# Performance work log

Measured on AMD Instinct MI355X. Metric: run time of the kernel, lower is better.

## Reference

```python
import jax, jax.numpy as jnp
import numpy as np

R = 3.0            # search_range
EPS = 0.01         # forward_backward_error
UPD_MULT = 1.0     # UPDATE_MULTIPLIER_THRESHOLD


def _clamp(coords, H, W):
    # coords [..., 2] = (x, y); clamp x to [0, W-1], y to [0, H-1]
    return jnp.stack([jnp.clip(coords[..., 0], 0.0, W - 1.0),
                      jnp.clip(coords[..., 1], 0.0, H - 1.0)], axis=-1)


def _scores(coords, corr_flat):
    # coords [B,H,W,2] (x,y); corr_flat [B*H*W, Hc, Wc]; bilinear sample one scalar per pixel
    B, H, W, _ = coords.shape
    N, Hc, Wc = corr_flat.shape
    c = coords.reshape(-1, 2)
    x, y = c[:, 0], c[:, 1]
    x0 = jnp.floor(x); y0 = jnp.floor(y)
    wx = x - x0; wy = y - y0
    x0i = jnp.clip(x0.astype(jnp.int32), 0, Wc - 1)
    x1i = jnp.clip(x0i + 1, 0, Wc - 1)
    y0i = jnp.clip(y0.astype(jnp.int32), 0, Hc - 1)
    y1i = jnp.clip(y0i + 1, 0, Hc - 1)
    n = jnp.arange(N)
    v00 = corr_flat[n, y0i, x0i]; v01 = corr_flat[n, y0i, x1i]
    v10 = corr_flat[n, y1i, x0i]; v11 = corr_flat[n, y1i, x1i]
    s = (v00 * (1 - wx) * (1 - wy) + v01 * wx * (1 - wy)
         + v10 * (1 - wx) * wy + v11 * wx * wy)
    return s.reshape(B, H, W)


def _propagate(coords, corr_flat, dxy):
    # PatchMatch propagation step along direction (dx, dy): take neighbor's match
    # shifted by the same pixel offset if it scores higher.
    dx, dy = dxy
    B, H, W, _ = coords.shape
    best = coords
    best_s = _scores(best, corr_flat)
    cand_h = _clamp(jnp.roll(coords, dx, axis=2) + jnp.array([dx, 0.0], coords.dtype), H, W)
    cand_v = _clamp(jnp.roll(coords, dy, axis=1) + jnp.array([0.0, dy], coords.dtype), H, W)
    for cand in (cand_h, cand_v):
        s = _scores(cand, corr_flat)
        upd = s > best_s
        best = jnp.where(upd[..., None], cand, best)
        best_s = jnp.maximum(s, best_s)
    return best


def _random_search(coords, corr_flat, key):
    B, H, W, _ = coords.shape
    new = _clamp(coords + R * jax.random.normal(key, coords.shape, coords.dtype), H, W)
    old_s = _scores(coords, corr_flat)
    new_s = _scores(new, corr_flat)
    upd = (new_s - UPD_MULT * old_s) > 0
    return jnp.where(upd[..., None], new, coords)


def _handle(matching, corr_flat, key):
    coords = jnp.transpose(matching, (0, 2, 3, 1))  # [B,H,W,2]
    k1, k2, k3 = jax.random.split(key, 3)
    res = _propagate(coords, corr_flat, (1, 1))
    res = _random_search(res, corr_flat, k1)
    res = _propagate(res, corr_flat, (-1, -1))
    res = _random_search(res, corr_flat, k2)
    res = _propagate(res, corr_flat, (-1, 1))
    res = _random_search(res, corr_flat, k3)
    res = _propagate(res, corr_flat, (1, -1))
    return res


def _bilinear_map(img, coords):
    # img [B,H,W,C] sampled at coords [B,H,W,2] (x,y) -> [B,H,W,C]
    B, H, W, C = img.shape
    def per_b(im, co):
        x = co[..., 0].reshape(-1); y = co[..., 1].reshape(-1)
        x0 = jnp.floor(x); y0 = jnp.floor(y)
        wx = (x - x0)[:, None]; wy = (y - y0)[:, None]
        x0i = jnp.clip(x0.astype(jnp.int32), 0, W - 1)
        x1i = jnp.clip(x0i + 1, 0, W - 1)
        y0i = jnp.clip(y0.astype(jnp.int32), 0, H - 1)
        y1i = jnp.clip(y0i + 1, 0, H - 1)
        v00 = im[y0i, x0i]; v01 = im[y0i, x1i]
        v10 = im[y1i, x0i]; v11 = im[y1i, x1i]
        out = (v00 * (1 - wx) * (1 - wy) + v01 * wx * (1 - wy)
               + v10 * (1 - wx) * wy + v11 * wx * wy)
        return out.reshape(H, W, C)
    return jax.vmap(per_b)(img, coords)


def setup_inputs() -> dict:
    key = jax.random.key(0)
    k1, k2, k3 = jax.random.split(key, 3)
    B, H, W = 4, 64, 64
    # matching fields: absolute (x, y) coords in-range
    mf = jax.random.uniform(k1, (B, 2, H, W), jnp.float32)
    mb = jax.random.uniform(k2, (B, 2, H, W), jnp.float32)
    scale = jnp.array([W - 1.0, H - 1.0], jnp.float32).reshape(1, 2, 1, 1)
    matching_f = mf * scale
    matching_b = mb * scale
    corr_map = jax.random.normal(k3, (B, H, W, H, W), jnp.float32)
    return {"matching_f": matching_f, "matching_b": matching_b, "corr_map": corr_map}


def reference(matching_f, matching_b, corr_map):
    B, H, W = corr_map.shape[0], corr_map.shape[1], corr_map.shape[2]
    corr_f = corr_map.reshape(B * H * W, H, W)
    # backward direction samples the transposed correlation volume
    corr_b = jnp.transpose(corr_map, (0, 3, 4, 1, 2)).reshape(B * H * W, H, W)
    key = jax.random.key(42)
    kf, kb = jax.random.split(key)
    res_f = _handle(matching_f, corr_f, kf)   # [B,H,W,2]
    res_b = _handle(matching_b, corr_b, kb)   # [B,H,W,2]
    # forward-backward consistency: sample backward field at forward matches
    counter = _bilinear_map(res_b, res_f)
    diff = jnp.max(jnp.abs(res_f - counter), axis=-1)
    invalid = (diff > EPS)[..., None]
    res = jnp.where(invalid, jnp.transpose(matching_f, (0, 2, 3, 1)), res_f)
    return jnp.transpose(res, (0, 3, 1, 2))
```

## Files before the change

### kernel.cpp

```cpp
#include <hip/hip_runtime.h>
#include <stdint.h>

#pragma clang fp contract(off)

__host__ __device__ inline void tf2x32(uint32_t k0, uint32_t k1,
                                       uint32_t x0, uint32_t x1,
                                       uint32_t* o0, uint32_t* o1) {
  const uint32_t ks2 = k0 ^ k1 ^ 0x1BD11BDAu;
  x0 += k0; x1 += k1;
#define TF_R(r) { x0 += x1; x1 = (x1 << (r)) | (x1 >> (32 - (r))); x1 ^= x0; }
  TF_R(13) TF_R(15) TF_R(26) TF_R(6)
  x0 += k1;  x1 += ks2 + 1u;
  TF_R(17) TF_R(29) TF_R(16) TF_R(24)
  x0 += ks2; x1 += k0 + 2u;
  TF_R(13) TF_R(15) TF_R(26) TF_R(6)
  x0 += k0;  x1 += k1 + 3u;
  TF_R(17) TF_R(29) TF_R(16) TF_R(24)
  x0 += k1;  x1 += ks2 + 4u;
  TF_R(13) TF_R(15) TF_R(26) TF_R(6)
  x0 += ks2; x1 += k0 + 5u;
#undef TF_R
  *o0 = x0; *o1 = x1;
}

__device__ inline float erfinv_xla(float x) {
#pragma clang fp contract(off)
  float w = -log1pf(-(x * x));
  float p;
  if (w < 5.0f) {
    w = w - 2.5f;
    p = 2.81022636e-08f;
    p = 3.43273939e-07f  + p * w;
    p = -3.5233877e-06f  + p * w;
    p = -4.39150654e-06f + p * w;
    p = 0.00021858087f   + p * w;
    p = -0.00125372503f  + p * w;
    p = -0.00417768164f  + p * w;
    p = 0.246640727f     + p * w;
    p = 1.50140941f      + p * w;
  } else {
    w = sqrtf(w) - 3.0f;
    p = -0.000200214257f;
    p = 0.000100950558f  + p * w;
    p = 0.00134934322f   + p * w;
    p = -0.00367342844f  + p * w;
    p = 0.00573950773f   + p * w;
    p = -0.0076224613f   + p * w;
    p = 0.00943887047f   + p * w;
    p = 1.00167406f      + p * w;
    p = 2.83297682f      + p * w;
  }
  return p * x;
}

__device__ inline float jax_normal(uint32_t k0, uint32_t k1, uint32_t idx) {
#pragma clang fp contract(off)
  uint32_t o0, o1;
  tf2x32(k0, k1, 0u, idx, &o0, &o1);
  uint32_t bits = o0 ^ o1;
  float f = __uint_as_float((bits >> 9) | 0x3f800000u) - 1.0f;
  float u = f * 2.0f + (-0x1.fffffep-1f);
  u = fmaxf(-0x1.fffffep-1f, u);
  return 0x1.6a09e6p+0f * erfinv_xla(u);
}

__device__ inline float score_at(const float* __restrict__ base, int stride,
                                 float x, float y) {
#pragma clang fp contract(off)
  float x0 = floorf(x), y0 = floorf(y);
  float wx = x - x0, wy = y - y0;
  int xi = (int)x0; xi = xi < 0 ? 0 : (xi > 63 ? 63 : xi);
  int yi = (int)y0; yi = yi < 0 ? 0 : (yi > 63 ? 63 : yi);
  int x1 = xi + 1 > 63 ? 63 : xi + 1;
  int y1 = yi + 1 > 63 ? 63 : yi + 1;
  float v00 = base[(yi * 64 + xi) * stride];
  float v01 = base[(yi * 64 + x1) * stride];
  float v10 = base[(y1 * 64 + xi) * stride];
  float v11 = base[(y1 * 64 + x1) * stride];
  float omx = 1.0f - wx, omy = 1.0f - wy;
  return (((v00 * omx) * omy + (v01 * wx) * omy) + (v10 * omx) * wy) + (v11 * wx) * wy;
}

__global__ __launch_bounds__(64) void step_kernel(
    const float* __restrict__ mf, const float* __restrict__ mb,
    const float4* __restrict__ in_c, float4* __restrict__ out_c,
    const float* __restrict__ corr, int dx, int dy,
    uint32_t k0f, uint32_t k1f, uint32_t k0b, uint32_t k1b,
    int do_rs, int from_matching) {
#pragma clang fp contract(off)
  int g = (int)(blockIdx.x * 64 + threadIdx.x);
  int dir = g >> 14, b = (g >> 12) & 3, p = g & 4095;
  int i = p >> 6, j = p & 63;

  const float* base; int stride;
  if (dir == 0) { base = corr + (size_t)(b * 4096 + p) * 4096; stride = 1; }
  else          { base = corr + (size_t)b * 16777216 + p;      stride = 4096; }

  int jh = (j - dx) & 63;
  int iv = (i - dy) & 63;

  float2 bst; float bs;
  float2 ch, cv;
  if (from_matching) {
    const float* m = dir ? mb : mf;
    float2 c = make_float2(m[((b * 2 + 0) * 64 + i) * 64 + j],
                           m[((b * 2 + 1) * 64 + i) * 64 + j]);
    ch = make_float2(m[((b * 2 + 0) * 64 + i ) * 64 + jh], m[((b * 2 + 1) * 64 + i ) * 64 + jh]);
    cv = make_float2(m[((b * 2 + 0) * 64 + iv) * 64 + j ], m[((b * 2 + 1) * 64 + iv) * 64 + j ]);
    bst = c;
    bs = score_at(base, stride, c.x, c.y);
  } else {
    const float4* ic = in_c + dir * 16384 + b * 4096;
    float4 own = ic[p];
    float4 nh  = ic[(i << 6) | jh];
    float4 nv  = ic[(iv << 6) | j];
    bst = make_float2(own.x, own.y);
    bs  = own.z;
    ch = make_float2(nh.x, nh.y);
    cv = make_float2(nv.x, nv.y);
  }
  ch.x = fminf(fmaxf(ch.x + (float)dx, 0.0f), 63.0f);
  cv.y = fminf(fmaxf(cv.y + (float)dy, 0.0f), 63.0f);

  float sh = score_at(base, stride, ch.x, ch.y);
  float sv = score_at(base, stride, cv.x, cv.y);
  if (sh > bs) bst = ch;
  bs = fmaxf(sh, bs);
  if (sv > bs) bst = cv;
  bs = fmaxf(sv, bs);

  if (do_rs) {
    uint32_t kk0 = dir ? k0b : k0f, kk1 = dir ? k1b : k1f;
    uint32_t pg = (uint32_t)(b * 4096 + p);
    float n0 = jax_normal(kk0, kk1, 2u * pg);
    float n1 = jax_normal(kk0, kk1, 2u * pg + 1u);
    float nx = fminf(fmaxf(bst.x + 3.0f * n0, 0.0f), 63.0f);
    float ny = fminf(fmaxf(bst.y + 3.0f * n1, 0.0f), 63.0f);
    float sn = score_at(base, stride, nx, ny);
    if (sn - bs > 0.0f) { bst = make_float2(nx, ny); bs = sn; }
  }
  out_c[dir * 16384 + b * 4096 + p] = make_float4(bst.x, bst.y, bs, 0.0f);
}

__global__ __launch_bounds__(256) void combine_kernel(const float* __restrict__ mf,
                                                      const float4* __restrict__ res,
                                                      float* __restrict__ out) {
#pragma clang fp contract(off)
  int pg = (int)(blockIdx.x * 256 + threadIdx.x);
  int b = pg >> 12, hw = pg & 4095;
  int i = hw >> 6, j = hw & 63;
  float4 rf4 = res[pg];
  float2 rf = make_float2(rf4.x, rf4.y);
  const float4* rb = res + 16384 + b * 4096;
  float x0 = floorf(rf.x), y0 = floorf(rf.y);
  float wx = rf.x - x0, wy = rf.y - y0;
  int xi = (int)x0; xi = xi < 0 ? 0 : (xi > 63 ? 63 : xi);
  int yi = (int)y0; yi = yi < 0 ? 0 : (yi > 63 ? 63 : yi);
  int x1 = xi + 1 > 63 ? 63 : xi + 1;
  int y1 = yi + 1 > 63 ? 63 : yi + 1;
  float4 v00 = rb[yi * 64 + xi], v01 = rb[yi * 64 + x1];
  float4 v10 = rb[y1 * 64 + xi], v11 = rb[y1 * 64 + x1];
  float omx = 1.0f - wx, omy = 1.0f - wy;
  float c0 = (((v00.x * omx) * omy + (v01.x * wx) * omy) + (v10.x * omx) * wy) + (v11.x * wx) * wy;
  float c1 = (((v00.y * omx) * omy + (v01.y * wx) * omy) + (v10.y * omx) * wy) + (v11.y * wx) * wy;
  float d = fmaxf(fabsf(rf.x - c0), fabsf(rf.y - c1));
  bool invalid = d > 0.01f;
  out[((b * 2 + 0) * 64 + i) * 64 + j] = invalid ? mf[((b * 2 + 0) * 64 + i) * 64 + j] : rf.x;
  out[((b * 2 + 1) * 64 + i) * 64 + j] = invalid ? mf[((b * 2 + 1) * 64 + i) * 64 + j] : rf.y;
}

extern "C" void kernel_launch(void* const* d_in, const int* in_sizes, int n_in,
                              void* d_out, int out_size, void* d_ws, size_t ws_size,
                              hipStream_t stream) {
  const float* mf   = (const float*)d_in[0];
  const float* mb   = (const float*)d_in[1];
  const float* corr = (const float*)d_in[2];
  float* out  = (float*)d_out;
  float4* bufA = (float4*)d_ws;
  float4* bufB = bufA + 32768;

  uint32_t kf0, kf1, kb0, kb1, K[12];
  tf2x32(0u, 42u, 0u, 0u, &kf0, &kf1);
  tf2x32(0u, 42u, 0u, 1u, &kb0, &kb1);
  for (uint32_t s = 0; s < 3; ++s) {
    tf2x32(kf0, kf1, 0u, s, &K[0 + s * 2], &K[0 + s * 2 + 1]);
    tf2x32(kb0, kb1, 0u, s, &K[6 + s * 2], &K[6 + s * 2 + 1]);
  }

  dim3 grid(512), block(64);
  step_kernel<<<grid, block, 0, stream>>>(mf, mb, nullptr, bufA, corr,  1,  1,
                                          K[0], K[1], K[6], K[7], 1, 1);
  step_kernel<<<grid, block, 0, stream>>>(mf, mb, bufA, bufB, corr, -1, -1,
                                          K[2], K[3], K[8], K[9], 1, 0);
  step_kernel<<<grid, block, 0, stream>>>(mf, mb, bufB, bufA, corr, -1,  1,
                                          K[4], K[5], K[10], K[11], 1, 0);
  step_kernel<<<grid, block, 0, stream>>>(mf, mb, bufA, bufB, corr,  1, -1,
                                          0u, 0u, 0u, 0u, 0, 0);
  combine_kernel<<<dim3(64), dim3(256), 0, stream>>>(mf, bufB, out);
  (void)in_sizes; (void)n_in; (void)out_size; (void)ws_size;
}
```

Measured before the change: 333.9 us.

## Fuse four propagation steps into one tiled kernel with halo recompute

Replaces the four sequential step kernel launches with a single kernel. Each 64-thread block handles an 8x8 tile and recomputes a shrinking halo (11x11, 10x10, 9x9) in shared memory, so the propagation stages need no global round trips or extra launches. This removes three launches and the intermediate buffer traffic. In exchange it does redundant scoring and RNG work on the halo pixels (121+100+81 vs 64 per stage), all of which do random gathers from the correlation volume. The intermediate result also shrinks from float4 to float2 for the combine step.

```diff
diff --git a/kernel.cpp b/kernel.cpp
--- a/kernel.cpp
+++ b/kernel.cpp
@@ -81,85 +81,141 @@
   return (((v00 * omx) * omy + (v01 * wx) * omy) + (v10 * omx) * wy) + (v11 * wx) * wy;
 }
 
-__global__ __launch_bounds__(64) void step_kernel(
-    const float* __restrict__ mf, const float* __restrict__ mb,
-    const float4* __restrict__ in_c, float4* __restrict__ out_c,
-    const float* __restrict__ corr, int dx, int dy,
-    uint32_t k0f, uint32_t k1f, uint32_t k0b, uint32_t k1b,
-    int do_rs, int from_matching) {
-#pragma clang fp contract(off)
-  int g = (int)(blockIdx.x * 64 + threadIdx.x);
-  int dir = g >> 14, b = (g >> 12) & 3, p = g & 4095;
-  int i = p >> 6, j = p & 63;
-
-  const float* base; int stride;
-  if (dir == 0) { base = corr + (size_t)(b * 4096 + p) * 4096; stride = 1; }
-  else          { base = corr + (size_t)b * 16777216 + p;      stride = 4096; }
-
-  int jh = (j - dx) & 63;
-  int iv = (i - dy) & 63;
-
-  float2 bst; float bs;
-  float2 ch, cv;
-  if (from_matching) {
-    const float* m = dir ? mb : mf;
-    float2 c = make_float2(m[((b * 2 + 0) * 64 + i) * 64 + j],
-                           m[((b * 2 + 1) * 64 + i) * 64 + j]);
-    ch = make_float2(m[((b * 2 + 0) * 64 + i ) * 64 + jh], m[((b * 2 + 1) * 64 + i ) * 64 + jh]);
-    cv = make_float2(m[((b * 2 + 0) * 64 + iv) * 64 + j ], m[((b * 2 + 1) * 64 + iv) * 64 + j ]);
-    bst = c;
-    bs = score_at(base, stride, c.x, c.y);
-  } else {
-    const float4* ic = in_c + dir * 16384 + b * 4096;
-    float4 own = ic[p];
-    float4 nh  = ic[(i << 6) | jh];
-    float4 nv  = ic[(iv << 6) | j];
-    bst = make_float2(own.x, own.y);
-    bs  = own.z;
-    ch = make_float2(nh.x, nh.y);
-    cv = make_float2(nv.x, nv.y);
-  }
-  ch.x = fminf(fmaxf(ch.x + (float)dx, 0.0f), 63.0f);
-  cv.y = fminf(fmaxf(cv.y + (float)dy, 0.0f), 63.0f);
-
-  float sh = score_at(base, stride, ch.x, ch.y);
-  float sv = score_at(base, stride, cv.x, cv.y);
-  if (sh > bs) bst = ch;
+__device__ inline float4 prop_rs(float2 own, float own_s, float2 nh, float2 nv,
+                                 float fdx, float fdy,
+                                 const float* __restrict__ base, int stride,
+                                 bool do_rs, uint32_t k0, uint32_t k1,
+                                 uint32_t pg) {
+#pragma clang fp contract(off)
+  float chx = fminf(fmaxf(nh.x + fdx, 0.0f), 63.0f);
+  float chy = nh.y;
+  float cvx = nv.x;
+  float cvy = fminf(fmaxf(nv.y + fdy, 0.0f), 63.0f);
+  float2 bst = own; float bs = own_s;
+  float sh = score_at(base, stride, chx, chy);
+  float sv = score_at(base, stride, cvx, cvy);
+  if (sh > bs) bst = make_float2(chx, chy);
   bs = fmaxf(sh, bs);
-  if (sv > bs) bst = cv;
+  if (sv > bs) bst = make_float2(cvx, cvy);
   bs = fmaxf(sv, bs);
-
   if (do_rs) {
-    uint32_t kk0 = dir ? k0b : k0f, kk1 = dir ? k1b : k1f;
-    uint32_t pg = (uint32_t)(b * 4096 + p);
-    float n0 = jax_normal(kk0, kk1, 2u * pg);
-    float n1 = jax_normal(kk0, kk1, 2u * pg + 1u);
+    float n0 = jax_normal(k0, k1, 2u * pg);
+    float n1 = jax_normal(k0, k1, 2u * pg + 1u);
     float nx = fminf(fmaxf(bst.x + 3.0f * n0, 0.0f), 63.0f);
     float ny = fminf(fmaxf(bst.y + 3.0f * n1, 0.0f), 63.0f);
     float sn = score_at(base, stride, nx, ny);
     if (sn - bs > 0.0f) { bst = make_float2(nx, ny); bs = sn; }
   }
-  out_c[dir * 16384 + b * 4096 + p] = make_float4(bst.x, bst.y, bs, 0.0f);
+  return make_float4(bst.x, bst.y, bs, 0.0f);
+}
+
+__global__ __launch_bounds__(64) void fused_kernel(
+    const float* __restrict__ mf, const float* __restrict__ mb,
+    const float* __restrict__ corr, float2* __restrict__ res,
+    uint32_t f10, uint32_t f11, uint32_t f20, uint32_t f21,
+    uint32_t f30, uint32_t f31,
+    uint32_t b10, uint32_t b11, uint32_t b20, uint32_t b21,
+    uint32_t b30, uint32_t b31) {
+#pragma clang fp contract(off)
+  const int bx  = (int)blockIdx.x;
+  const int dir = bx >> 8;
+  const int b   = (bx >> 6) & 3;
+  const int tile = bx & 63;
+  const int i0 = (tile >> 3) << 3;
+  const int j0 = (tile & 7) << 3;
+  const int tid = (int)threadIdx.x;
+
+  const float* __restrict__ m = dir ? mb : mf;
+  const uint32_t k10 = dir ? b10 : f10, k11 = dir ? b11 : f11;
+  const uint32_t k20 = dir ? b20 : f20, k21 = dir ? b21 : f21;
+  const uint32_t k30 = dir ? b30 : f30, k31 = dir ? b31 : f31;
+  const int    stride  = dir ? 4096 : 1;
+  const size_t pstride = dir ? 1 : 4096;
+  const float* __restrict__ corrb = corr + (size_t)b * 16777216u;
+  const float* __restrict__ mx = m + (size_t)((b * 2 + 0) * 64) * 64;
+  const float* __restrict__ my = m + (size_t)((b * 2 + 1) * 64) * 64;
+
+  __shared__ float4 S1[121];
+  __shared__ float4 S2[100];
+  __shared__ float4 S3[81];
+
+  for (int idx = tid; idx < 121; idx += 64) {
+    int r = idx / 11, c = idx - r * 11;
+    int ii = (i0 - 1 + r) & 63, jj = (j0 - 1 + c) & 63;
+    int p = (ii << 6) | jj;
+    const float* base = corrb + (size_t)p * pstride;
+    int jh = (jj - 1) & 63, iv = (ii - 1) & 63;
+    float2 own = make_float2(mx[(ii << 6) | jj], my[(ii << 6) | jj]);
+    float2 nh  = make_float2(mx[(ii << 6) | jh], my[(ii << 6) | jh]);
+    float2 nv  = make_float2(mx[(iv << 6) | jj], my[(iv << 6) | jj]);
+    float own_s = score_at(base, stride, own.x, own.y);
+    S1[idx] = prop_rs(own, own_s, nh, nv, 1.0f, 1.0f, base, stride,
+                      true, k10, k11, (uint32_t)((b << 12) | p));
+  }
+  __syncthreads();
+
+  for (int idx = tid; idx < 100; idx += 64) {
+    int r = idx / 10, c = idx - r * 10;
+    int ii = (i0 - 1 + r) & 63, jj = (j0 - 1 + c) & 63;
+    int p = (ii << 6) | jj;
+    const float* base = corrb + (size_t)p * pstride;
+    float4 o = S1[r * 11 + c];
+    float4 h = S1[r * 11 + c + 1];
+    float4 v = S1[(r + 1) * 11 + c];
+    S2[idx] = prop_rs(make_float2(o.x, o.y), o.z,
+                      make_float2(h.x, h.y), make_float2(v.x, v.y),
+                      -1.0f, -1.0f, base, stride,
+                      true, k20, k21, (uint32_t)((b << 12) | p));
+  }
+  __syncthreads();
+
+  for (int idx = tid; idx < 81; idx += 64) {
+    int r = idx / 9, c = idx - r * 9;
+    int ii = (i0 + r) & 63, jj = (j0 - 1 + c) & 63;
+    int p = (ii << 6) | jj;
+    const float* base = corrb + (size_t)p * pstride;
+    float4 o = S2[(r + 1) * 10 + c];
+    float4 h = S2[(r + 1) * 10 + c + 1];
+    float4 v = S2[r * 10 + c];
+    S3[idx] = prop_rs(make_float2(o.x, o.y), o.z,
+                      make_float2(h.x, h.y), make_float2(v.x, v.y),
+                      -1.0f, 1.0f, base, stride,
+                      true, k30, k31, (uint32_t)((b << 12) | p));
+  }
+  __syncthreads();
+
+  {
+    int r = tid >> 3, c = tid & 7;
+    int ii = i0 + r, jj = j0 + c;
+    int p = (ii << 6) | jj;
+    const float* base = corrb + (size_t)p * pstride;
+    float4 o = S3[r * 9 + c + 1];
+    float4 h = S3[r * 9 + c];
+    float4 v = S3[(r + 1) * 9 + c + 1];
+    float4 fin = prop_rs(make_float2(o.x, o.y), o.z,
+                         make_float2(h.x, h.y), make_float2(v.x, v.y),
+                         1.0f, -1.0f, base, stride, false, 0u, 0u, 0u);
+    res[(dir << 14) | (b << 12) | p] = make_float2(fin.x, fin.y);
+  }
 }
 
 __global__ __launch_bounds__(256) void combine_kernel(const float* __restrict__ mf,
-                                                      const float4* __restrict__ res,
+                                                      const float2* __restrict__ res,
                                                       float* __restrict__ out) {
 #pragma clang fp contract(off)
   int pg = (int)(blockIdx.x * 256 + threadIdx.x);
   int b = pg >> 12, hw = pg & 4095;
   int i = hw >> 6, j = hw & 63;
-  float4 rf4 = res[pg];
-  float2 rf = make_float2(rf4.x, rf4.y);
-  const float4* rb = res + 16384 + b * 4096;
+  float2 rf = res[pg];
+  const float2* rb = res + 16384 + (b << 12);
   float x0 = floorf(rf.x), y0 = floorf(rf.y);
   float wx = rf.x - x0, wy = rf.y - y0;
   int xi = (int)x0; xi = xi < 0 ? 0 : (xi > 63 ? 63 : xi);
   int yi = (int)y0; yi = yi < 0 ? 0 : (yi > 63 ? 63 : yi);
   int x1 = xi + 1 > 63 ? 63 : xi + 1;
   int y1 = yi + 1 > 63 ? 63 : yi + 1;
-  float4 v00 = rb[yi * 64 + xi], v01 = rb[yi * 64 + x1];
-  float4 v10 = rb[y1 * 64 + xi], v11 = rb[y1 * 64 + x1];
+  float2 v00 = rb[yi * 64 + xi], v01 = rb[yi * 64 + x1];
+  float2 v10 = rb[y1 * 64 + xi], v11 = rb[y1 * 64 + x1];
   float omx = 1.0f - wx, omy = 1.0f - wy;
   float c0 = (((v00.x * omx) * omy + (v01.x * wx) * omy) + (v10.x * omx) * wy) + (v11.x * wx) * wy;
   float c1 = (((v00.y * omx) * omy + (v01.y * wx) * omy) + (v10.y * omx) * wy) + (v11.y * wx) * wy;
@@ -176,8 +232,7 @@
   const float* mb   = (const float*)d_in[1];
   const float* corr = (const float*)d_in[2];
   float* out  = (float*)d_out;
-  float4* bufA = (float4*)d_ws;
-  float4* bufB = bufA + 32768;
+  float2* res = (float2*)d_ws;
 
   uint32_t kf0, kf1, kb0, kb1, K[12];
   tf2x32(0u, 42u, 0u, 0u, &kf0, &kf1);
@@ -187,15 +242,10 @@
     tf2x32(kb0, kb1, 0u, s, &K[6 + s * 2], &K[6 + s * 2 + 1]);
   }
 
-  dim3 grid(512), block(64);
-  step_kernel<<<grid, block, 0, stream>>>(mf, mb, nullptr, bufA, corr,  1,  1,
-                                          K[0], K[1], K[6], K[7], 1, 1);
-  step_kernel<<<grid, block, 0, stream>>>(mf, mb, bufA, bufB, corr, -1, -1,
-                                          K[2], K[3], K[8], K[9], 1, 0);
-  step_kernel<<<grid, block, 0, stream>>>(mf, mb, bufB, bufA, corr, -1,  1,
-                                          K[4], K[5], K[10], K[11], 1, 0);
-  step_kernel<<<grid, block, 0, stream>>>(mf, mb, bufA, bufB, corr,  1, -1,
-                                          0u, 0u, 0u, 0u, 0, 0);
-  combine_kernel<<<dim3(64), dim3(256), 0, stream>>>(mf, bufB, out);
+  fused_kernel<<<dim3(512), dim3(64), 0, stream>>>(
+      mf, mb, corr, res,
+      K[0], K[1], K[2], K[3], K[4], K[5],
+      K[6], K[7], K[8], K[9], K[10], K[11]);
+  combine_kernel<<<dim3(64), dim3(256), 0, stream>>>(mf, res, out);
   (void)in_sizes; (void)n_in; (void)out_size; (void)ws_size;
 }
```

Measured after the change: 328.4 us. No clear change (-1.6%).
